# Performance work log

Measured on AMD Instinct MI355X. Metric: run time of the kernel, lower is better.

The kernel has to match this reference:

```python
import jax, jax.numpy as jnp
import numpy as np

B = 16384
LATENT = 64
COND = 6
H = 256
OUT = 3
NUM_LAYERS = 2
IN0 = OUT + LATENT + COND  # 73, LSTM layer-0 input size


def setup_inputs() -> dict:
    key = jax.random.key(0)
    ks = jax.random.split(key, 16)
    s = 0.05
    return {
        "z": jax.random.normal(ks[0], (B, LATENT), jnp.float32),
        "conditions": jax.random.normal(ks[1], (B, COND), jnp.float32),
        "fc_init_w": jax.random.normal(ks[2], (H * NUM_LAYERS, LATENT + COND), jnp.float32) * s,
        "fc_init_b": jax.random.normal(ks[3], (H * NUM_LAYERS,), jnp.float32) * s,
        "w_ih0": jax.random.normal(ks[4], (4 * H, IN0), jnp.float32) * s,
        "w_hh0": jax.random.normal(ks[5], (4 * H, H), jnp.float32) * s,
        "b_ih0": jax.random.normal(ks[6], (4 * H,), jnp.float32) * s,
        "b_hh0": jax.random.normal(ks[7], (4 * H,), jnp.float32) * s,
        "w_ih1": jax.random.normal(ks[8], (4 * H, H), jnp.float32) * s,
        "w_hh1": jax.random.normal(ks[9], (4 * H, H), jnp.float32) * s,
        "b_ih1": jax.random.normal(ks[10], (4 * H,), jnp.float32) * s,
        "b_hh1": jax.random.normal(ks[11], (4 * H,), jnp.float32) * s,
        "out_w1": jax.random.normal(ks[12], (H // 2, H), jnp.float32) * s,
        "out_b1": jax.random.normal(ks[13], (H // 2,), jnp.float32) * s,
        "out_w2": jax.random.normal(ks[14], (OUT, H // 2), jnp.float32) * s,
        "out_b2": jax.random.normal(ks[15], (OUT,), jnp.float32) * s,
        "seq_len": 50,
    }


def _lstm_cell(x, h, c, w_ih, w_hh, b_ih, b_hh):
    # PyTorch gate order: i, f, g, o
    gates = x @ w_ih.T + b_ih + h @ w_hh.T + b_hh  # [B, 4H]
    i, f, g, o = jnp.split(gates, 4, axis=-1)
    c_new = jax.nn.sigmoid(f) * c + jax.nn.sigmoid(i) * jnp.tanh(g)
    h_new = jax.nn.sigmoid(o) * jnp.tanh(c_new)
    return h_new, c_new


def reference(z, conditions, fc_init_w, fc_init_b,
              w_ih0, w_hh0, b_ih0, b_hh0,
              w_ih1, w_hh1, b_ih1, b_hh1,
              out_w1, out_b1, out_w2, out_b2, seq_len):
    batch = z.shape[0]
    zc = jnp.concatenate([z, conditions], axis=1)  # [B, latent+cond]
    init_h = (zc @ fc_init_w.T + fc_init_b).reshape(batch, NUM_LAYERS, H)
    h0, h1 = init_h[:, 0, :], init_h[:, 1, :]
    c0 = jnp.zeros_like(h0)
    c1 = jnp.zeros_like(h1)
    cur = conditions[:, :3]  # start waypoint as first input

    def step(carry, _):
        h0, c0, h1, c1, cur = carry
        x = jnp.concatenate([cur, z, conditions], axis=1)  # [B, IN0]
        h0n, c0n = _lstm_cell(x, h0, c0, w_ih0, w_hh0, b_ih0, b_hh0)
        h1n, c1n = _lstm_cell(h0n, h1, c1, w_ih1, w_hh1, b_ih1, b_hh1)
        hid = jax.nn.relu(h1n @ out_w1.T + out_b1)
        out = hid @ out_w2.T + out_b2  # [B, 3]
        return (h0n, c0n, h1n, c1n, out), out

    _, ys = jax.lax.scan(step, (h0, c0, h1, c1, cur), None, length=seq_len)
    return jnp.transpose(ys, (1, 0, 2))  # [B, seq_len, 3]
```

## Files before the change

### kernel.cpp

```cpp
#include <hip/hip_runtime.h>
#include <hip/hip_bf16.h>

typedef short short8 __attribute__((ext_vector_type(8)));
typedef float f32x4 __attribute__((ext_vector_type(4)));

#define BROWS 64
#define NTHR  512
#define XK    96
#define XSTR  104
#define HSTR  264
#define HIDSTR 129
#define NKT0  11
#define NKT1  16
#define NKTO  8
#define PK0_ELEMS (64*NKT0*512)
#define PK1_ELEMS (64*NKT1*512)
#define PKO_ELEMS (8*NKTO*512)

#define L_X    0
#define L_H    13312
#define HBUF   (BROWS*HSTR)
#define HBUF_B (HBUF*2)
#define L_HID  (L_H + 3*HBUF_B)
#define L_OW2  (L_HID + BROWS*HIDSTR*4)
#define L_OB2  (L_OW2 + 1536)
#define LDS_TOTAL 149264

__device__ inline unsigned short f2bf(float x){
  unsigned u = __float_as_uint(x);
  u += 0x7FFFu + ((u >> 16) & 1u);
  return (unsigned short)(u >> 16);
}
__device__ inline float bf2f(unsigned short s){ return __uint_as_float(((unsigned)s) << 16); }
__device__ inline float sigm(float x){ return 1.f / (1.f + __expf(-x)); }
__device__ inline float ftanh(float x){ float e = __expf(2.f*x); return 1.f - 2.f/(e + 1.f); }

__global__ void pack_weights(const float* __restrict__ wih0, const float* __restrict__ whh0,
                             const float* __restrict__ bih0, const float* __restrict__ bhh0,
                             const float* __restrict__ wih1, const float* __restrict__ whh1,
                             const float* __restrict__ ow1,
                             unsigned short* __restrict__ wsb){
  int idx = blockIdx.x * blockDim.x + threadIdx.x;
  int total = PK0_ELEMS + PK1_ELEMS + PKO_ELEMS;
  if (idx >= total) return;
  float w;
  size_t off;
  if (idx < PK0_ELEMS) {
    int nt = idx / (NKT0*512), rem = idx % (NKT0*512), kt = rem / 512, li = rem % 512;
    int lane = li >> 3, j = li & 7;
    int n = lane & 15, k = ((lane >> 4) << 3) + j;
    int Kg = kt*32 + k, g = nt*16 + n;
    if (Kg < 73)        w = wih0[g*73 + Kg];
    else if (Kg == 73)  w = bih0[g] + bhh0[g];
    else if (Kg < XK)   w = 0.f;
    else                w = whh0[g*256 + (Kg - XK)];
    off = ((size_t)(nt*NKT0 + kt)*64 + lane)*8 + j;
  } else if (idx < PK0_ELEMS + PK1_ELEMS) {
    int i2 = idx - PK0_ELEMS;
    int nt = i2 / (NKT1*512), rem = i2 % (NKT1*512), kt = rem / 512, li = rem % 512;
    int lane = li >> 3, j = li & 7;
    int n = lane & 15, k = ((lane >> 4) << 3) + j;
    int Kg = kt*32 + k, g = nt*16 + n;
    w = (Kg < 256) ? wih1[g*256 + Kg] : whh1[g*256 + (Kg - 256)];
    off = (size_t)PK0_ELEMS + ((size_t)(nt*NKT1 + kt)*64 + lane)*8 + j;
  } else {
    int i2 = idx - PK0_ELEMS - PK1_ELEMS;
    int nt = i2 / (NKTO*512), rem = i2 % (NKTO*512), kt = rem / 512, li = rem % 512;
    int lane = li >> 3, j = li & 7;
    int n = lane & 15, k = ((lane >> 4) << 3) + j;
    int Kg = kt*32 + k, uh = nt*16 + n;
    w = ow1[uh*256 + Kg];
    off = (size_t)PK0_ELEMS + (size_t)PK1_ELEMS + ((size_t)(nt*NKTO + kt)*64 + lane)*8 + j;
  }
  wsb[off] = f2bf(w);
}

__global__ void __launch_bounds__(NTHR)
__attribute__((amdgpu_num_vgpr(256)))
traj_main(const float* __restrict__ z, const float* __restrict__ cond,
          const float* __restrict__ fiw, const float* __restrict__ fib,
          const float* __restrict__ bih1, const float* __restrict__ bhh1,
          const float* __restrict__ ob1,  const float* __restrict__ ow2,
          const float* __restrict__ ob2,
          const unsigned short* __restrict__ wsb, const int* __restrict__ seqp,
          float* __restrict__ out){
  __shared__ __align__(16) char smem[LDS_TOTAL];
  unsigned short* Xl  = (unsigned short*)(smem + L_X);
  unsigned short* Hl  = (unsigned short*)(smem + L_H);
  float*          HIDl= (float*)(smem + L_HID);
  float*          OW2l= (float*)(smem + L_OW2);
  float*          OB2l= (float*)(smem + L_OB2);

  const int tid = threadIdx.x, wv = tid >> 6, lane = tid & 63;
  const int bid = blockIdx.x;
  const int row0 = bid * BROWS;
  const int T = *seqp;

  const unsigned short* pk0i = wsb;
  const unsigned short* pk1i = wsb + (size_t)PK0_ELEMS;
  const unsigned short* pkoi = wsb + (size_t)PK0_ELEMS + (size_t)PK1_ELEMS;

  {
    int r = tid >> 3, seg = tid & 7;
    int gr = row0 + r;
    for (int c = seg*13; c < seg*13 + 13; ++c) {
      float v;
      if (c < 3)        v = cond[gr*6 + c];
      else if (c < 67)  v = z[gr*64 + (c - 3)];
      else if (c < 73)  v = cond[gr*6 + (c - 67)];
      else if (c == 73) v = 1.0f;
      else              v = 0.f;
      Xl[r*XSTR + c] = f2bf(v);
    }
  }
  if (tid < 384) OW2l[tid] = ow2[tid];
  if (tid < 3)   OB2l[tid] = ob2[tid];

  {
    int r = tid >> 3, ub = (tid & 7) * 32;
    int gr = row0 + r;
    #pragma unroll 1
    for (int u = ub; u < ub + 32; ++u) {
      float s0 = fib[u], s1 = fib[256 + u];
      const float* w0r = fiw + (size_t)u * 70;
      const float* w1r = fiw + (size_t)(256 + u) * 70;
      for (int jj = 0; jj < 64; ++jj) { float xv = z[gr*64 + jj]; s0 += xv * w0r[jj]; s1 += xv * w1r[jj]; }
      for (int jj = 0; jj < 6;  ++jj) { float xv = cond[gr*6 + jj]; s0 += xv * w0r[64 + jj]; s1 += xv * w1r[64 + jj]; }
      Hl[0*HBUF + r*HSTR + u] = f2bf(s0);
      Hl[1*HBUF + r*HSTR + u] = f2bf(s1);
    }
  }

  float bias1r[8];
  #pragma unroll
  for (int p = 0; p < 2; ++p) {
    int u = wv*32 + p*16 + (lane & 15);
    #pragma unroll
    for (int g = 0; g < 4; ++g)
      bias1r[p*4 + g] = bih1[g*256 + u] + bhh1[g*256 + u];
  }
  float ob1r = ob1[wv*16 + (lane & 15)];

  float c0s[32], c1s[32];
  #pragma unroll
  for (int i = 0; i < 32; ++i) { c0s[i] = 0.f; c1s[i] = 0.f; }

  __syncthreads();

  const int arow = lane & 15, koff = (lane >> 4) * 8;

  int ia = 0, ib = 1, ic = 2;

  for (int t = 0; t < T; ++t) {
    const unsigned short* Ha = Hl + ia*HBUF;
    const unsigned short* Hb = Hl + ib*HBUF;
    unsigned short*       Hc = Hl + ic*HBUF;
    unsigned short*       HaW= Hl + ia*HBUF;

    #pragma unroll
    for (int p = 0; p < 2; ++p) {
      const unsigned short* wb = pk0i + ((size_t)((wv*2 + p)*NKT0)*64 + lane)*8;

      short8 wh[2][4];
      #pragma unroll
      for (int g = 0; g < 4; ++g)
        wh[0][g] = *(const short8*)(wb + (size_t)g*(16*NKT0*512));

      f32x4 acc[4][4];
      #pragma unroll
      for (int mt = 0; mt < 4; ++mt)
        #pragma unroll
        for (int g = 0; g < 4; ++g) acc[mt][g] = (f32x4){0.f, 0.f, 0.f, 0.f};

      #pragma unroll
      for (int kt = 0; kt < NKT0; ++kt) {
        const int cb = kt & 1, nb = cb ^ 1;
        if (kt + 1 < NKT0) {
          #pragma unroll
          for (int g = 0; g < 4; ++g)
            wh[nb][g] = *(const short8*)(wb + (size_t)g*(16*NKT0*512) + (size_t)(kt+1)*512);
        }
        short8 a[4];
        if (kt < 3) {
          #pragma unroll
          for (int mt = 0; mt < 4; ++mt)
            a[mt] = *(const short8*)(Xl + (mt*16 + arow)*XSTR + kt*32 + koff);
        } else {
          #pragma unroll
          for (int mt = 0; mt < 4; ++mt)
            a[mt] = *(const short8*)(Ha + (mt*16 + arow)*HSTR + (kt - 3)*32 + koff);
        }
        #pragma unroll
        for (int g = 0; g < 4; ++g)
          #pragma unroll
          for (int mt = 0; mt < 4; ++mt)
            acc[mt][g] = __builtin_amdgcn_mfma_f32_16x16x32_bf16(a[mt], wh[cb][g], acc[mt][g], 0, 0, 0);
      }

      const int u = wv*32 + p*16 + (lane & 15);
      #pragma unroll
      for (int mt = 0; mt < 4; ++mt) {
        #pragma unroll
        for (int q = 0; q < 4; ++q) {
          float iv = sigm(acc[mt][0][q]);
          float fv = sigm(acc[mt][1][q]);
          float gv = ftanh(acc[mt][2][q]);
          float ov = sigm(acc[mt][3][q]);
          float cn = fv * c0s[(p*4 + mt)*4 + q] + iv * gv;
          c0s[(p*4 + mt)*4 + q] = cn;
          float hn = ov * ftanh(cn);
          int r = mt*16 + ((lane >> 4) << 2) + q;
          Hc[r*HSTR + u] = f2bf(hn);
        }
      }
    }
    __syncthreads();

    #pragma unroll
    for (int p = 0; p < 2; ++p) {
      const unsigned short* wb = pk1i + ((size_t)((wv*2 + p)*NKT1)*64 + lane)*8;

      short8 wh[2][4];
      #pragma unroll
      for (int g = 0; g < 4; ++g)
        wh[0][g] = *(const short8*)(wb + (size_t)g*(16*NKT1*512));

      f32x4 acc[4][4];
      #pragma unroll
      for (int mt = 0; mt < 4; ++mt)
        #pragma unroll
        for (int g = 0; g < 4; ++g) {
          float b = bias1r[p*4 + g];
          acc[mt][g] = (f32x4){b, b, b, b};
        }

      #pragma unroll
      for (int kt = 0; kt < NKT1; ++kt) {
        const int cb = kt & 1, nb = cb ^ 1;
        if (kt + 1 < NKT1) {
          #pragma unroll
          for (int g = 0; g < 4; ++g)
            wh[nb][g] = *(const short8*)(wb + (size_t)g*(16*NKT1*512) + (size_t)(kt+1)*512);
        }
        short8 a[4];
        if (kt < 8) {
          #pragma unroll
          for (int mt = 0; mt < 4; ++mt)
            a[mt] = *(const short8*)(Hc + (mt*16 + arow)*HSTR + kt*32 + koff);
        } else {
          #pragma unroll
          for (int mt = 0; mt < 4; ++mt)
            a[mt] = *(const short8*)(Hb + (mt*16 + arow)*HSTR + (kt - 8)*32 + koff);
        }
        #pragma unroll
        for (int g = 0; g < 4; ++g)
          #pragma unroll
          for (int mt = 0; mt < 4; ++mt)
            acc[mt][g] = __builtin_amdgcn_mfma_f32_16x16x32_bf16(a[mt], wh[cb][g], acc[mt][g], 0, 0, 0);
      }

      const int u = wv*32 + p*16 + (lane & 15);
      #pragma unroll
      for (int mt = 0; mt < 4; ++mt) {
        #pragma unroll
        for (int q = 0; q < 4; ++q) {
          float iv = sigm(acc[mt][0][q]);
          float fv = sigm(acc[mt][1][q]);
          float gv = ftanh(acc[mt][2][q]);
          float ov = sigm(acc[mt][3][q]);
          float cn = fv * c1s[(p*4 + mt)*4 + q] + iv * gv;
          c1s[(p*4 + mt)*4 + q] = cn;
          float hn = ov * ftanh(cn);
          int r = mt*16 + ((lane >> 4) << 2) + q;
          HaW[r*HSTR + u] = f2bf(hn);
        }
      }
    }
    __syncthreads();

    {
      const unsigned short* wb = pkoi + ((size_t)(wv*NKTO)*64 + lane)*8;
      short8 wh[2];
      wh[0] = *(const short8*)(wb);

      f32x4 acc3[4];
      #pragma unroll
      for (int mt = 0; mt < 4; ++mt) acc3[mt] = (f32x4){ob1r, ob1r, ob1r, ob1r};

      #pragma unroll
      for (int kt = 0; kt < NKTO; ++kt) {
        const int cb = kt & 1, nb = cb ^ 1;
        if (kt + 1 < NKTO)
          wh[nb] = *(const short8*)(wb + (size_t)(kt+1)*512);
        short8 a[4];
        #pragma unroll
        for (int mt = 0; mt < 4; ++mt)
          a[mt] = *(const short8*)(HaW + (mt*16 + arow)*HSTR + kt*32 + koff);
        #pragma unroll
        for (int mt = 0; mt < 4; ++mt)
          acc3[mt] = __builtin_amdgcn_mfma_f32_16x16x32_bf16(a[mt], wh[cb], acc3[mt], 0, 0, 0);
      }
      const int uh = wv*16 + (lane & 15);
      #pragma unroll
      for (int mt = 0; mt < 4; ++mt)
        #pragma unroll
        for (int q = 0; q < 4; ++q) {
          float hv = fmaxf(acc3[mt][q], 0.f);
          int r = mt*16 + ((lane >> 4) << 2) + q;
          HIDl[r*HIDSTR + uh] = hv;
        }
    }
    __syncthreads();

    {
      int r = tid >> 3, e = tid & 7;
      const float* hrow = HIDl + r*HIDSTR + e*16;
      float s0 = 0.f, s1 = 0.f, s2 = 0.f;
      #pragma unroll
      for (int k = 0; k < 16; ++k) {
        float hv = hrow[k];
        int kk = e*16 + k;
        s0 += hv * OW2l[kk];
        s1 += hv * OW2l[128 + kk];
        s2 += hv * OW2l[256 + kk];
      }
      #pragma unroll
      for (int d = 4; d; d >>= 1) {
        s0 += __shfl_down(s0, d, 8);
        s1 += __shfl_down(s1, d, 8);
        s2 += __shfl_down(s2, d, 8);
      }
      if (e == 0) {
        s0 += OB2l[0]; s1 += OB2l[1]; s2 += OB2l[2];
        int gr = row0 + r;
        float* orow = out + (size_t)gr * (T*3) + t*3;
        orow[0] = s0; orow[1] = s1; orow[2] = s2;
        Xl[r*XSTR + 0] = f2bf(s0);
        Xl[r*XSTR + 1] = f2bf(s1);
        Xl[r*XSTR + 2] = f2bf(s2);
      }
    }
    __syncthreads();

    int tmp = ia; ia = ic; ic = ib; ib = tmp;
  }
}

extern "C" void kernel_launch(void* const* d_in, const int* in_sizes, int n_in,
                              void* d_out, int out_size, void* d_ws, size_t ws_size,
                              hipStream_t stream){
  const float* z    = (const float*)d_in[0];
  const float* cond = (const float*)d_in[1];
  const float* fiw  = (const float*)d_in[2];
  const float* fib  = (const float*)d_in[3];
  const float* wih0 = (const float*)d_in[4];
  const float* whh0 = (const float*)d_in[5];
  const float* bih0 = (const float*)d_in[6];
  const float* bhh0 = (const float*)d_in[7];
  const float* wih1 = (const float*)d_in[8];
  const float* whh1 = (const float*)d_in[9];
  const float* bih1 = (const float*)d_in[10];
  const float* bhh1 = (const float*)d_in[11];
  const float* ow1  = (const float*)d_in[12];
  const float* ob1  = (const float*)d_in[13];
  const float* ow2  = (const float*)d_in[14];
  const float* ob2  = (const float*)d_in[15];
  const int*   seqp = (const int*)d_in[16];
  unsigned short* wsb = (unsigned short*)d_ws;
  float* outp = (float*)d_out;

  int packtot = PK0_ELEMS + PK1_ELEMS + PKO_ELEMS;
  pack_weights<<<(packtot + 255)/256, 256, 0, stream>>>(wih0, whh0, bih0, bhh0,
                                                        wih1, whh1, ow1, wsb);
  traj_main<<<16384/BROWS, NTHR, 0, stream>>>(z, cond, fiw, fib,
                                              bih1, bhh1,
                                              ob1, ow2, ob2, wsb, seqp, outp);
}
```

Measured before the change: 5.712 ms.

## Spill LSTM cell state to global workspace and drop weight double-buffering

After: 7.619 ms. +33.4%, slower.

```diff
diff --git a/kernel.cpp b/kernel.cpp
--- a/kernel.cpp
+++ b/kernel.cpp
@@ -16,6 +16,10 @@
 #define PK0_ELEMS (64*NKT0*512)
 #define PK1_ELEMS (64*NKT1*512)
 #define PKO_ELEMS (8*NKTO*512)
+
+#define CWS_OFF_BYTES (2*1024*1024)
+#define CWS_FLOATS ((size_t)256*4*4*NTHR*4)
+#define WS_NEED (CWS_OFF_BYTES + CWS_FLOATS*4)
 
 #define L_X    0
 #define L_H    13312
@@ -75,15 +79,15 @@
   wsb[off] = f2bf(w);
 }
 
+template<int CWS>
 __global__ void __launch_bounds__(NTHR)
-__attribute__((amdgpu_num_vgpr(256)))
 traj_main(const float* __restrict__ z, const float* __restrict__ cond,
           const float* __restrict__ fiw, const float* __restrict__ fib,
           const float* __restrict__ bih1, const float* __restrict__ bhh1,
           const float* __restrict__ ob1,  const float* __restrict__ ow2,
           const float* __restrict__ ob2,
-          const unsigned short* __restrict__ wsb, const int* __restrict__ seqp,
-          float* __restrict__ out){
+          const unsigned short* __restrict__ wsb, float* __restrict__ cws,
+          const int* __restrict__ seqp, float* __restrict__ out){
   __shared__ __align__(16) char smem[LDS_TOTAL];
   unsigned short* Xl  = (unsigned short*)(smem + L_X);
   unsigned short* Hl  = (unsigned short*)(smem + L_H);
@@ -141,9 +145,11 @@
   }
   float ob1r = ob1[wv*16 + (lane & 15)];
 
-  float c0s[32], c1s[32];
-  #pragma unroll
-  for (int i = 0; i < 32; ++i) { c0s[i] = 0.f; c1s[i] = 0.f; }
+  float c0s[CWS ? 1 : 32], c1s[CWS ? 1 : 32];
+  if constexpr (!CWS) {
+    #pragma unroll
+    for (int i = 0; i < 32; ++i) { c0s[i] = 0.f; c1s[i] = 0.f; }
+  }
 
   __syncthreads();
 
@@ -161,10 +167,14 @@
     for (int p = 0; p < 2; ++p) {
       const unsigned short* wb = pk0i + ((size_t)((wv*2 + p)*NKT0)*64 + lane)*8;
 
-      short8 wh[2][4];
-      #pragma unroll
-      for (int g = 0; g < 4; ++g)
-        wh[0][g] = *(const short8*)(wb + (size_t)g*(16*NKT0*512));
+      f32x4 cc[4];
+      if constexpr (CWS) {
+        const int pc = p;
+        #pragma unroll
+        for (int i4 = 0; i4 < 4; ++i4)
+          cc[i4] = __builtin_nontemporal_load(
+              (const f32x4*)(cws + ((((size_t)bid*4 + pc)*4 + i4)*NTHR + tid)*4));
+      }
 
       f32x4 acc[4][4];
       #pragma unroll
@@ -174,12 +184,10 @@
 
       #pragma unroll
       for (int kt = 0; kt < NKT0; ++kt) {
-        const int cb = kt & 1, nb = cb ^ 1;
-        if (kt + 1 < NKT0) {
-          #pragma unroll
-          for (int g = 0; g < 4; ++g)
-            wh[nb][g] = *(const short8*)(wb + (size_t)g*(16*NKT0*512) + (size_t)(kt+1)*512);
-        }
+        short8 w[4];
+        #pragma unroll
+        for (int g = 0; g < 4; ++g)
+          w[g] = *(const short8*)(wb + (size_t)g*(16*NKT0*512) + (size_t)kt*512);
         short8 a[4];
         if (kt < 3) {
           #pragma unroll
@@ -194,7 +202,7 @@
         for (int g = 0; g < 4; ++g)
           #pragma unroll
           for (int mt = 0; mt < 4; ++mt)
-            acc[mt][g] = __builtin_amdgcn_mfma_f32_16x16x32_bf16(a[mt], wh[cb][g], acc[mt][g], 0, 0, 0);
+            acc[mt][g] = __builtin_amdgcn_mfma_f32_16x16x32_bf16(a[mt], w[g], acc[mt][g], 0, 0, 0);
       }
 
       const int u = wv*32 + p*16 + (lane & 15);
@@ -206,13 +214,21 @@
           float fv = sigm(acc[mt][1][q]);
           float gv = ftanh(acc[mt][2][q]);
           float ov = sigm(acc[mt][3][q]);
-          float cn = fv * c0s[(p*4 + mt)*4 + q] + iv * gv;
-          c0s[(p*4 + mt)*4 + q] = cn;
+          float cold = CWS ? cc[mt][q] : c0s[(p*4 + mt)*4 + q];
+          float cn = fv * cold + iv * gv;
+          if constexpr (CWS) cc[mt][q] = cn; else c0s[(p*4 + mt)*4 + q] = cn;
           float hn = ov * ftanh(cn);
           int r = mt*16 + ((lane >> 4) << 2) + q;
           Hc[r*HSTR + u] = f2bf(hn);
         }
       }
+      if constexpr (CWS) {
+        const int pc = p;
+        #pragma unroll
+        for (int i4 = 0; i4 < 4; ++i4)
+          __builtin_nontemporal_store(cc[i4],
+              (f32x4*)(cws + ((((size_t)bid*4 + pc)*4 + i4)*NTHR + tid)*4));
+      }
     }
     __syncthreads();
 
@@ -220,10 +236,14 @@
     for (int p = 0; p < 2; ++p) {
       const unsigned short* wb = pk1i + ((size_t)((wv*2 + p)*NKT1)*64 + lane)*8;
 
-      short8 wh[2][4];
-      #pragma unroll
-      for (int g = 0; g < 4; ++g)
-        wh[0][g] = *(const short8*)(wb + (size_t)g*(16*NKT1*512));
+      f32x4 cc[4];
+      if constexpr (CWS) {
+        const int pc = 2 + p;
+        #pragma unroll
+        for (int i4 = 0; i4 < 4; ++i4)
+          cc[i4] = __builtin_nontemporal_load(
+              (const f32x4*)(cws + ((((size_t)bid*4 + pc)*4 + i4)*NTHR + tid)*4));
+      }
 
       f32x4 acc[4][4];
       #pragma unroll
@@ -236,12 +256,10 @@
 
       #pragma unroll
       for (int kt = 0; kt < NKT1; ++kt) {
-        const int cb = kt & 1, nb = cb ^ 1;
-        if (kt + 1 < NKT1) {
-          #pragma unroll
-          for (int g = 0; g < 4; ++g)
-            wh[nb][g] = *(const short8*)(wb + (size_t)g*(16*NKT1*512) + (size_t)(kt+1)*512);
-        }
+        short8 w[4];
+        #pragma unroll
+        for (int g = 0; g < 4; ++g)
+          w[g] = *(const short8*)(wb + (size_t)g*(16*NKT1*512) + (size_t)kt*512);
         short8 a[4];
         if (kt < 8) {
           #pragma unroll
@@ -256,7 +274,7 @@
         for (int g = 0; g < 4; ++g)
           #pragma unroll
           for (int mt = 0; mt < 4; ++mt)
-            acc[mt][g] = __builtin_amdgcn_mfma_f32_16x16x32_bf16(a[mt], wh[cb][g], acc[mt][g], 0, 0, 0);
+            acc[mt][g] = __builtin_amdgcn_mfma_f32_16x16x32_bf16(a[mt], w[g], acc[mt][g], 0, 0, 0);
       }
 
       const int u = wv*32 + p*16 + (lane & 15);
@@ -268,37 +286,40 @@
           float fv = sigm(acc[mt][1][q]);
           float gv = ftanh(acc[mt][2][q]);
           float ov = sigm(acc[mt][3][q]);
-          float cn = fv * c1s[(p*4 + mt)*4 + q] + iv * gv;
-          c1s[(p*4 + mt)*4 + q] = cn;
+          float cold = CWS ? cc[mt][q] : c1s[(p*4 + mt)*4 + q];
+          float cn = fv * cold + iv * gv;
+          if constexpr (CWS) cc[mt][q] = cn; else c1s[(p*4 + mt)*4 + q] = cn;
           float hn = ov * ftanh(cn);
           int r = mt*16 + ((lane >> 4) << 2) + q;
           HaW[r*HSTR + u] = f2bf(hn);
         }
       }
+      if constexpr (CWS) {
+        const int pc = 2 + p;
+        #pragma unroll
+        for (int i4 = 0; i4 < 4; ++i4)
+          __builtin_nontemporal_store(cc[i4],
+              (f32x4*)(cws + ((((size_t)bid*4 + pc)*4 + i4)*NTHR + tid)*4));
+      }
     }
     __syncthreads();
 
     {
       const unsigned short* wb = pkoi + ((size_t)(wv*NKTO)*64 + lane)*8;
-      short8 wh[2];
-      wh[0] = *(const short8*)(wb);
-
       f32x4 acc3[4];
       #pragma unroll
       for (int mt = 0; mt < 4; ++mt) acc3[mt] = (f32x4){ob1r, ob1r, ob1r, ob1r};
 
       #pragma unroll
       for (int kt = 0; kt < NKTO; ++kt) {
-        const int cb = kt & 1, nb = cb ^ 1;
-        if (kt + 1 < NKTO)
-          wh[nb] = *(const short8*)(wb + (size_t)(kt+1)*512);
+        const short8 bw = *(const short8*)(wb + (size_t)kt*512);
         short8 a[4];
         #pragma unroll
         for (int mt = 0; mt < 4; ++mt)
           a[mt] = *(const short8*)(HaW + (mt*16 + arow)*HSTR + kt*32 + koff);
         #pragma unroll
         for (int mt = 0; mt < 4; ++mt)
-          acc3[mt] = __builtin_amdgcn_mfma_f32_16x16x32_bf16(a[mt], wh[cb], acc3[mt], 0, 0, 0);
+          acc3[mt] = __builtin_amdgcn_mfma_f32_16x16x32_bf16(a[mt], bw, acc3[mt], 0, 0, 0);
       }
       const int uh = wv*16 + (lane & 15);
       #pragma unroll
@@ -372,7 +393,13 @@
   int packtot = PK0_ELEMS + PK1_ELEMS + PKO_ELEMS;
   pack_weights<<<(packtot + 255)/256, 256, 0, stream>>>(wih0, whh0, bih0, bhh0,
                                                         wih1, whh1, ow1, wsb);
-  traj_main<<<16384/BROWS, NTHR, 0, stream>>>(z, cond, fiw, fib,
-                                              bih1, bhh1,
-                                              ob1, ow2, ob2, wsb, seqp, outp);
+  if (ws_size >= WS_NEED) {
+    float* cws = (float*)((char*)d_ws + CWS_OFF_BYTES);
+    hipMemsetAsync(cws, 0, CWS_FLOATS*4, stream);
+    traj_main<1><<<16384/BROWS, NTHR, 0, stream>>>(z, cond, fiw, fib, bih1, bhh1,
+                                                   ob1, ow2, ob2, wsb, cws, seqp, outp);
+  } else {
+    traj_main<0><<<16384/BROWS, NTHR, 0, stream>>>(z, cond, fiw, fib, bih1, bhh1,
+                                                   ob1, ow2, ob2, wsb, nullptr, seqp, outp);
+  }
 }
```

## Stream packed LSTM weights through per-wave LDS ring via global_load_lds

Applied to the files above, without the earlier changes.

Result: slower. 6.542 ms (+14.5%).

```diff
diff --git a/kernel.cpp b/kernel.cpp
--- a/kernel.cpp
+++ b/kernel.cpp
@@ -9,7 +9,7 @@
 #define XK    96
 #define XSTR  104
 #define HSTR  264
-#define HIDSTR 129
+#define HID2STR 136
 #define NKT0  11
 #define NKT1  16
 #define NKTO  8
@@ -21,10 +21,17 @@
 #define L_H    13312
 #define HBUF   (BROWS*HSTR)
 #define HBUF_B (HBUF*2)
-#define L_HID  (L_H + 3*HBUF_B)
-#define L_OW2  (L_HID + BROWS*HIDSTR*4)
+#define L_OW2  (L_H + 3*HBUF_B)
 #define L_OB2  (L_OW2 + 1536)
-#define LDS_TOTAL 149264
+#define L_RING (L_OB2 + 16)
+#define LDS_TOTAL (L_RING + 8*5*1024)
+
+#define WAITVM(N) { constexpr int _n=(N); \
+  if constexpr(_n<=0)      asm volatile("s_waitcnt vmcnt(0)":::"memory"); \
+  else if constexpr(_n==1) asm volatile("s_waitcnt vmcnt(1)":::"memory"); \
+  else if constexpr(_n==2) asm volatile("s_waitcnt vmcnt(2)":::"memory"); \
+  else                     asm volatile("s_waitcnt vmcnt(3)":::"memory"); }
+#define LGKM0 asm volatile("s_waitcnt lgkmcnt(0)":::"memory")
 
 __device__ inline unsigned short f2bf(float x){
   unsigned u = __float_as_uint(x);
@@ -34,6 +41,12 @@
 __device__ inline float bf2f(unsigned short s){ return __uint_as_float(((unsigned)s) << 16); }
 __device__ inline float sigm(float x){ return 1.f / (1.f + __expf(-x)); }
 __device__ inline float ftanh(float x){ float e = __expf(2.f*x); return 1.f - 2.f/(e + 1.f); }
+
+__device__ __forceinline__ void stage16(const unsigned short* g, unsigned short* l){
+  __builtin_amdgcn_global_load_lds(
+      (const __attribute__((address_space(1))) unsigned int*)g,
+      (__attribute__((address_space(3))) unsigned int*)l, 16, 0, 0);
+}
 
 __global__ void pack_weights(const float* __restrict__ wih0, const float* __restrict__ whh0,
                              const float* __restrict__ bih0, const float* __restrict__ bhh0,
@@ -76,7 +89,6 @@
 }
 
 __global__ void __launch_bounds__(NTHR)
-__attribute__((amdgpu_num_vgpr(256)))
 traj_main(const float* __restrict__ z, const float* __restrict__ cond,
           const float* __restrict__ fiw, const float* __restrict__ fib,
           const float* __restrict__ bih1, const float* __restrict__ bhh1,
@@ -87,7 +99,6 @@
   __shared__ __align__(16) char smem[LDS_TOTAL];
   unsigned short* Xl  = (unsigned short*)(smem + L_X);
   unsigned short* Hl  = (unsigned short*)(smem + L_H);
-  float*          HIDl= (float*)(smem + L_HID);
   float*          OW2l= (float*)(smem + L_OW2);
   float*          OB2l= (float*)(smem + L_OB2);
 
@@ -99,6 +110,7 @@
   const unsigned short* pk0i = wsb;
   const unsigned short* pk1i = wsb + (size_t)PK0_ELEMS;
   const unsigned short* pkoi = wsb + (size_t)PK0_ELEMS + (size_t)PK1_ELEMS;
+  unsigned short* RGu = (unsigned short*)(smem + L_RING) + (size_t)wv*(5*512);
 
   {
     int r = tid >> 3, seg = tid & 7;
@@ -156,15 +168,17 @@
     const unsigned short* Hb = Hl + ib*HBUF;
     unsigned short*       Hc = Hl + ic*HBUF;
     unsigned short*       HaW= Hl + ia*HBUF;
+    unsigned short*       HIDb = Hl + ib*HBUF;
 
     #pragma unroll
     for (int p = 0; p < 2; ++p) {
-      const unsigned short* wb = pk0i + ((size_t)((wv*2 + p)*NKT0)*64 + lane)*8;
-
-      short8 wh[2][4];
-      #pragma unroll
-      for (int g = 0; g < 4; ++g)
-        wh[0][g] = *(const short8*)(wb + (size_t)g*(16*NKT0*512));
+      #define ISSUE_M1(nn) { \
+        constexpr int _kt = (nn) >> 1, _gp = (nn) & 1; \
+        stage16(pk0i + ((size_t)(((_gp*2+0)*16 + wv*2 + p)*NKT0 + _kt))*512 + lane*8, \
+                RGu + ((2*(nn)  ) % 5)*512); \
+        stage16(pk0i + ((size_t)(((_gp*2+1)*16 + wv*2 + p)*NKT0 + _kt))*512 + lane*8, \
+                RGu + ((2*(nn)+1) % 5)*512); }
+      ISSUE_M1(0); ISSUE_M1(1);
 
       f32x4 acc[4][4];
       #pragma unroll
@@ -174,12 +188,6 @@
 
       #pragma unroll
       for (int kt = 0; kt < NKT0; ++kt) {
-        const int cb = kt & 1, nb = cb ^ 1;
-        if (kt + 1 < NKT0) {
-          #pragma unroll
-          for (int g = 0; g < 4; ++g)
-            wh[nb][g] = *(const short8*)(wb + (size_t)g*(16*NKT0*512) + (size_t)(kt+1)*512);
-        }
         short8 a[4];
         if (kt < 3) {
           #pragma unroll
@@ -191,11 +199,29 @@
             a[mt] = *(const short8*)(Ha + (mt*16 + arow)*HSTR + (kt - 3)*32 + koff);
         }
         #pragma unroll
-        for (int g = 0; g < 4; ++g)
-          #pragma unroll
-          for (int mt = 0; mt < 4; ++mt)
-            acc[mt][g] = __builtin_amdgcn_mfma_f32_16x16x32_bf16(a[mt], wh[cb][g], acc[mt][g], 0, 0, 0);
-      }
+        for (int gp = 0; gp < 2; ++gp) {
+          const int n = kt*2 + gp;
+          if (n < 2*NKT0 - 1) { WAITVM(2) } else { WAITVM(0) }
+          short8 w0 = *(const short8*)(RGu + ((2*n  ) % 5)*512 + lane*8);
+          short8 w1 = *(const short8*)(RGu + ((2*n+1) % 5)*512 + lane*8);
+          #pragma unroll
+          for (int mt = 0; mt < 4; ++mt)
+            acc[mt][gp*2+0] = __builtin_amdgcn_mfma_f32_16x16x32_bf16(a[mt], w0, acc[mt][gp*2+0], 0, 0, 0);
+          #pragma unroll
+          for (int mt = 0; mt < 4; ++mt)
+            acc[mt][gp*2+1] = __builtin_amdgcn_mfma_f32_16x16x32_bf16(a[mt], w1, acc[mt][gp*2+1], 0, 0, 0);
+          if (n + 2 < 2*NKT0) {
+            LGKM0;
+            const int m = n + 2;
+            const int mkt = m >> 1, mgp = m & 1;
+            stage16(pk0i + ((size_t)(((mgp*2+0)*16 + wv*2 + p)*NKT0 + mkt))*512 + lane*8,
+                    RGu + ((2*m  ) % 5)*512);
+            stage16(pk0i + ((size_t)(((mgp*2+1)*16 + wv*2 + p)*NKT0 + mkt))*512 + lane*8,
+                    RGu + ((2*m+1) % 5)*512);
+          }
+        }
+      }
+      #undef ISSUE_M1
 
       const int u = wv*32 + p*16 + (lane & 15);
       #pragma unroll
@@ -218,12 +244,13 @@
 
     #pragma unroll
     for (int p = 0; p < 2; ++p) {
-      const unsigned short* wb = pk1i + ((size_t)((wv*2 + p)*NKT1)*64 + lane)*8;
-
-      short8 wh[2][4];
-      #pragma unroll
-      for (int g = 0; g < 4; ++g)
-        wh[0][g] = *(const short8*)(wb + (size_t)g*(16*NKT1*512));
+      #define ISSUE_M2(nn) { \
+        constexpr int _kt = (nn) >> 1, _gp = (nn) & 1; \
+        stage16(pk1i + ((size_t)(((_gp*2+0)*16 + wv*2 + p)*NKT1 + _kt))*512 + lane*8, \
+                RGu + ((2*(nn)  ) % 5)*512); \
+        stage16(pk1i + ((size_t)(((_gp*2+1)*16 + wv*2 + p)*NKT1 + _kt))*512 + lane*8, \
+                RGu + ((2*(nn)+1) % 5)*512); }
+      ISSUE_M2(0); ISSUE_M2(1);
 
       f32x4 acc[4][4];
       #pragma unroll
@@ -236,12 +263,6 @@
 
       #pragma unroll
       for (int kt = 0; kt < NKT1; ++kt) {
-        const int cb = kt & 1, nb = cb ^ 1;
-        if (kt + 1 < NKT1) {
-          #pragma unroll
-          for (int g = 0; g < 4; ++g)
-            wh[nb][g] = *(const short8*)(wb + (size_t)g*(16*NKT1*512) + (size_t)(kt+1)*512);
-        }
         short8 a[4];
         if (kt < 8) {
           #pragma unroll
@@ -253,11 +274,29 @@
             a[mt] = *(const short8*)(Hb + (mt*16 + arow)*HSTR + (kt - 8)*32 + koff);
         }
         #pragma unroll
-        for (int g = 0; g < 4; ++g)
-          #pragma unroll
-          for (int mt = 0; mt < 4; ++mt)
-            acc[mt][g] = __builtin_amdgcn_mfma_f32_16x16x32_bf16(a[mt], wh[cb][g], acc[mt][g], 0, 0, 0);
-      }
+        for (int gp = 0; gp < 2; ++gp) {
+          const int n = kt*2 + gp;
+          if (n < 2*NKT1 - 1) { WAITVM(2) } else { WAITVM(0) }
+          short8 w0 = *(const short8*)(RGu + ((2*n  ) % 5)*512 + lane*8);
+          short8 w1 = *(const short8*)(RGu + ((2*n+1) % 5)*512 + lane*8);
+          #pragma unroll
+          for (int mt = 0; mt < 4; ++mt)
+            acc[mt][gp*2+0] = __builtin_amdgcn_mfma_f32_16x16x32_bf16(a[mt], w0, acc[mt][gp*2+0], 0, 0, 0);
+          #pragma unroll
+          for (int mt = 0; mt < 4; ++mt)
+            acc[mt][gp*2+1] = __builtin_amdgcn_mfma_f32_16x16x32_bf16(a[mt], w1, acc[mt][gp*2+1], 0, 0, 0);
+          if (n + 2 < 2*NKT1) {
+            LGKM0;
+            const int m = n + 2;
+            const int mkt = m >> 1, mgp = m & 1;
+            stage16(pk1i + ((size_t)(((mgp*2+0)*16 + wv*2 + p)*NKT1 + mkt))*512 + lane*8,
+                    RGu + ((2*m  ) % 5)*512);
+            stage16(pk1i + ((size_t)(((mgp*2+1)*16 + wv*2 + p)*NKT1 + mkt))*512 + lane*8,
+                    RGu + ((2*m+1) % 5)*512);
+          }
+        }
+      }
+      #undef ISSUE_M2
 
       const int u = wv*32 + p*16 + (lane & 15);
       #pragma unroll
@@ -279,9 +318,9 @@
     __syncthreads();
 
     {
-      const unsigned short* wb = pkoi + ((size_t)(wv*NKTO)*64 + lane)*8;
-      short8 wh[2];
-      wh[0] = *(const short8*)(wb);
+      #pragma unroll
+      for (int s = 0; s < 4; ++s)
+        stage16(pkoi + ((size_t)(wv*NKTO + s))*512 + lane*8, RGu + (s % 5)*512);
 
       f32x4 acc3[4];
       #pragma unroll
@@ -289,16 +328,22 @@
 
       #pragma unroll
       for (int kt = 0; kt < NKTO; ++kt) {
-        const int cb = kt & 1, nb = cb ^ 1;
-        if (kt + 1 < NKTO)
-          wh[nb] = *(const short8*)(wb + (size_t)(kt+1)*512);
+        if (kt < 5)      { WAITVM(3) }
+        else if (kt == 5){ WAITVM(2) }
+        else if (kt == 6){ WAITVM(1) }
+        else             { WAITVM(0) }
+        const short8 bw = *(const short8*)(RGu + (kt % 5)*512 + lane*8);
         short8 a[4];
         #pragma unroll
         for (int mt = 0; mt < 4; ++mt)
           a[mt] = *(const short8*)(HaW + (mt*16 + arow)*HSTR + kt*32 + koff);
         #pragma unroll
         for (int mt = 0; mt < 4; ++mt)
-          acc3[mt] = __builtin_amdgcn_mfma_f32_16x16x32_bf16(a[mt], wh[cb], acc3[mt], 0, 0, 0);
+          acc3[mt] = __builtin_amdgcn_mfma_f32_16x16x32_bf16(a[mt], bw, acc3[mt], 0, 0, 0);
+        if (kt + 4 < NKTO) {
+          LGKM0;
+          stage16(pkoi + ((size_t)(wv*NKTO + kt + 4))*512 + lane*8, RGu + ((kt + 4) % 5)*512);
+        }
       }
       const int uh = wv*16 + (lane & 15);
       #pragma unroll
@@ -307,18 +352,18 @@
         for (int q = 0; q < 4; ++q) {
           float hv = fmaxf(acc3[mt][q], 0.f);
           int r = mt*16 + ((lane >> 4) << 2) + q;
-          HIDl[r*HIDSTR + uh] = hv;
+          HIDb[r*HID2STR + uh] = f2bf(hv);
         }
     }
     __syncthreads();
 
     {
       int r = tid >> 3, e = tid & 7;
-      const float* hrow = HIDl + r*HIDSTR + e*16;
+      const unsigned short* hrow = HIDb + r*HID2STR + e*16;
       float s0 = 0.f, s1 = 0.f, s2 = 0.f;
       #pragma unroll
       for (int k = 0; k < 16; ++k) {
-        float hv = hrow[k];
+        float hv = bf2f(hrow[k]);
         int kk = e*16 + k;
         s0 += hv * OW2l[kk];
         s1 += hv * OW2l[128 + kk];
```
